# Kernel optimization log

Measured on AMD Instinct MI355X. Metric: run time of the kernel, lower is better.

## Reference

```python
import jax, jax.numpy as jnp
import numpy as np
from jax import lax

B, H, W, D_MODEL = 2, 64, 64, 96
EXPAND = 2
D_INNER = EXPAND * D_MODEL  # 192
D_STATE = 16
D_CONV = 3
DT_RANK = -(-D_MODEL // 16)  # 6 ('auto')
K = 2  # num_direction


def diagonal_order(size):
    # faithful to SCANS 'diagonal': main diag, then upper tri row-major, then lower tri
    locs = [i * size + i for i in range(size)]
    for i in range(size):
        for j in range(i + 1, size):
            locs.append(i * size + j)
    for i in range(size):
        for j in range(i):
            locs.append(i * size + j)
    return np.asarray(locs, dtype=np.int32)

_ORDER = diagonal_order(H)               # encode: gather by locs_flat
_INV_ORDER = np.argsort(_ORDER).astype(np.int32)  # decode: gather by argsort(locs_flat)


def setup_inputs():
    key = jax.random.key(0)
    ks = jax.random.split(key, 8)
    s = 0.02
    return {
        "x": jax.random.normal(ks[0], (B, H, W, D_MODEL), jnp.float32),
        "w_in": jax.random.normal(ks[1], (2 * D_INNER, D_MODEL), jnp.float32) * s,
        "conv_w": jax.random.normal(ks[2], (D_INNER, 1, D_CONV, D_CONV), jnp.float32) * 0.1,
        "conv_b": jnp.zeros((D_INNER,), jnp.float32),
        "x_proj_w": jax.random.normal(ks[3], (K, DT_RANK + 2 * D_STATE, D_INNER), jnp.float32) * s,
        "dt_w": jax.random.uniform(ks[4], (K, D_INNER, DT_RANK), jnp.float32, -(DT_RANK ** -0.5), DT_RANK ** -0.5),
        "dt_b": jax.random.uniform(ks[5], (K, D_INNER), jnp.float32, -4.6, -2.3),  # inv-softplus of dt in [~1e-2,1e-1]
        "A_logs": jnp.tile(jnp.log(jnp.arange(1, D_STATE + 1, dtype=jnp.float32))[None, :], (K * D_INNER, 1)),
        "Ds": jnp.ones((K * D_INNER,), jnp.float32),
        "ln_g": jnp.ones((D_INNER,), jnp.float32),
        "ln_b": jnp.zeros((D_INNER,), jnp.float32),
        "w_out": jax.random.normal(ks[6], (D_MODEL, D_INNER), jnp.float32) * s,
    }


def _selective_scan(xs, dts, A, Bs, Cs, Ds2, dt_bias):
    # xs, dts: (B,K,D,L); A: (K,D,N); Bs, Cs: (B,K,N,L); Ds2, dt_bias: (K,D)
    delta = jax.nn.softplus(dts + dt_bias[None, :, :, None])           # (B,K,D,L)
    dA = jnp.exp(jnp.einsum('bkdl,kdn->lbkdn', delta, A))              # (L,B,K,D,N)
    dBu = jnp.einsum('bkdl,bknl,bkdl->lbkdn', delta, Bs, xs)           # (L,B,K,D,N)
    Ct = jnp.transpose(Cs, (3, 0, 1, 2))                               # (L,B,K,N)

    h0 = jnp.zeros(dA.shape[1:], dA.dtype)                             # (B,K,D,N)

    def step(h, inp):
        a, bu, c = inp
        h = a * h + bu
        y = jnp.einsum('bkdn,bkn->bkd', h, c)
        return h, y

    _, ys = lax.scan(step, h0, (dA, dBu, Ct))                          # ys: (L,B,K,D)
    return jnp.transpose(ys, (1, 2, 3, 0)) + Ds2[None, :, :, None] * xs  # (B,K,D,L)


def reference(x, w_in, conv_w, conv_b, x_proj_w, dt_w, dt_b, A_logs, Ds, ln_g, ln_b, w_out):
    Bsz, Hh, Ww, _ = x.shape
    L = Hh * Ww
    order = jnp.asarray(_ORDER)
    inv = jnp.asarray(_INV_ORDER)

    xz = x @ w_in.T                                   # (B,H,W,2*D_INNER)
    xi, z = jnp.split(xz, 2, axis=-1)

    xc = jnp.transpose(xi, (0, 3, 1, 2))              # (B,D,H,W)
    xc = lax.conv_general_dilated(xc, conv_w, (1, 1), 'SAME',
                                  feature_group_count=D_INNER)
    xc = jax.nn.silu(xc + conv_b[None, :, None, None])

    xf = xc.reshape(Bsz, D_INNER, L)
    xs0 = xf[:, :, order]                             # diagonal-scan encode
    xs = jnp.stack([xs0, xs0[:, :, ::-1]], axis=1)    # (B,K,D,L), fwd + reversed

    x_dbl = jnp.einsum('bkdl,kcd->bkcl', xs, x_proj_w)
    dts, Bs, Cs = jnp.split(x_dbl, [DT_RANK, DT_RANK + D_STATE], axis=2)
    dts = jnp.einsum('bkrl,kdr->bkdl', dts, dt_w)

    A = -jnp.exp(A_logs).reshape(K, D_INNER, D_STATE)
    out_y = _selective_scan(xs, dts, A, Bs, Cs, Ds.reshape(K, D_INNER), dt_b)  # (B,K,D,L)

    y = out_y[:, 0] + out_y[:, 1, :, ::-1]            # un-flip reverse direction, merge
    y = y[:, :, inv]                                  # diagonal-scan decode
    y = jnp.transpose(y, (0, 2, 1)).reshape(Bsz, Hh, Ww, D_INNER)

    mu = jnp.mean(y, axis=-1, keepdims=True)
    var = jnp.var(y, axis=-1, keepdims=True)
    y = (y - mu) * lax.rsqrt(var + 1e-5) * ln_g + ln_b  # out_norm (LayerNorm)

    y = y * jax.nn.silu(z)
    return y @ w_out.T
```

## Files before the change

### kernel.cpp

```cpp
#include <hip/hip_runtime.h>
#include <math.h>

#define BB 2
#define DM 96
#define DI 192
#define DST 16
#define DRK 6
#define LL 4096
#define NCH 128
#define CT 32

__device__ __forceinline__ int inv_ord(int i, int j) {
    if (i == j) return i;
    if (j > i)  return 64 + i * 63 - (i * (i - 1)) / 2 + (j - i - 1);
    return 2080 + (i * (i - 1)) / 2 + j;
}

__device__ __forceinline__ float silu_f(float v) {
    return v / (1.f + __expf(-v));
}

__device__ __forceinline__ float softplus_f(float a) {
    return a > 20.f ? a : __logf(1.f + __expf(a));
}

__global__ __launch_bounds__(256) void k_gemm_in(const float* __restrict__ x,
                                                 const float* __restrict__ w_in,
                                                 float* __restrict__ xi,
                                                 float* __restrict__ zs) {
    __shared__ float aT[96][68];
    __shared__ float bT[96][68];
    const int tid = threadIdx.x;
    const int bm = blockIdx.x, bn = blockIdx.y;

    for (int f = tid; f < 64 * 24; f += 256) {
        int mm = f / 24, k4 = f % 24;
        float4 v = *(const float4*)(x + (size_t)(bm * 64 + mm) * 96 + k4 * 4);
        aT[k4 * 4 + 0][mm] = v.x; aT[k4 * 4 + 1][mm] = v.y;
        aT[k4 * 4 + 2][mm] = v.z; aT[k4 * 4 + 3][mm] = v.w;
    }
    for (int f = tid; f < 64 * 24; f += 256) {
        int nn = f / 24, k4 = f % 24;
        float4 v = *(const float4*)(w_in + (size_t)(bn * 64 + nn) * 96 + k4 * 4);
        bT[k4 * 4 + 0][nn] = v.x; bT[k4 * 4 + 1][nn] = v.y;
        bT[k4 * 4 + 2][nn] = v.z; bT[k4 * 4 + 3][nn] = v.w;
    }
    __syncthreads();

    const int tn = tid & 15, tm = tid >> 4;
    float acc[4][4] = {};
#pragma unroll 4
    for (int k = 0; k < 96; ++k) {
        float4 av = *(const float4*)&aT[k][tm * 4];
        float4 bv = *(const float4*)&bT[k][tn * 4];
        acc[0][0] += av.x * bv.x; acc[0][1] += av.x * bv.y; acc[0][2] += av.x * bv.z; acc[0][3] += av.x * bv.w;
        acc[1][0] += av.y * bv.x; acc[1][1] += av.y * bv.y; acc[1][2] += av.y * bv.z; acc[1][3] += av.y * bv.w;
        acc[2][0] += av.z * bv.x; acc[2][1] += av.z * bv.y; acc[2][2] += av.z * bv.z; acc[2][3] += av.z * bv.w;
        acc[3][0] += av.w * bv.x; acc[3][1] += av.w * bv.y; acc[3][2] += av.w * bv.z; acc[3][3] += av.w * bv.w;
    }

#pragma unroll
    for (int i = 0; i < 4; ++i) {
#pragma unroll
        for (int j = 0; j < 4; ++j) {
            int m = bm * 64 + tm * 4 + i;
            int n = bn * 64 + tn * 4 + j;
            float v = acc[i][j];
            if (n < DI) xi[(size_t)m * DI + n] = v;
            else        zs[(size_t)m * DI + (n - DI)] = silu_f(v);
        }
    }
}

__global__ __launch_bounds__(256) void k_conv(const float* __restrict__ xi,
                                              const float* __restrict__ cw,
                                              const float* __restrict__ cb,
                                              float* __restrict__ xs0) {
    int t = blockIdx.x * 256 + threadIdx.x;
    int c4 = t % 48;
    int p = t / 48;
    int b = p >> 12;
    int hw = p & 4095;
    int i = hw >> 6, j = hw & 63;
    int c = c4 * 4;
    float a0 = cb[c], a1 = cb[c + 1], a2 = cb[c + 2], a3 = cb[c + 3];
#pragma unroll
    for (int kh = -1; kh <= 1; ++kh) {
        int i2 = i + kh;
        if (i2 < 0 || i2 > 63) continue;
#pragma unroll
        for (int kw = -1; kw <= 1; ++kw) {
            int j2 = j + kw;
            if (j2 < 0 || j2 > 63) continue;
            float4 v = *(const float4*)(xi + ((size_t)(b << 12) + (i2 << 6) + j2) * DI + c);
            int wi = (kh + 1) * 3 + (kw + 1);
            a0 += v.x * cw[(c + 0) * 9 + wi];
            a1 += v.y * cw[(c + 1) * 9 + wi];
            a2 += v.z * cw[(c + 2) * 9 + wi];
            a3 += v.w * cw[(c + 3) * 9 + wi];
        }
    }
    a0 = silu_f(a0); a1 = silu_f(a1); a2 = silu_f(a2); a3 = silu_f(a3);
    int m = inv_ord(i, j);
    *(float4*)(xs0 + ((size_t)(b << 12) + m) * DI + c) = make_float4(a0, a1, a2, a3);
}

__global__ __launch_bounds__(512) void k_proj4(const float* __restrict__ xs0,
                                               const float* __restrict__ xpw,
                                               float* __restrict__ t) {
    __shared__ float xa[192 * 65];
    const int tid = threadIdx.x;
    const int rowbase = blockIdx.x * 64;
    const int k = blockIdx.y;

    for (int f = tid; f < 64 * 48; f += 512) {
        int r = f / 48, q4 = f % 48;
        float4 v = *(const float4*)(xs0 + (size_t)(rowbase + r) * DI + q4 * 4);
        xa[(q4 * 4 + 0) * 65 + r] = v.x;
        xa[(q4 * 4 + 1) * 65 + r] = v.y;
        xa[(q4 * 4 + 2) * 65 + r] = v.z;
        xa[(q4 * 4 + 3) * 65 + r] = v.w;
    }
    __syncthreads();

    const int w = __builtin_amdgcn_readfirstlane(tid >> 6);
    const int lane = tid & 63;
    const float* wb = xpw + (size_t)k * 38 * DI;

    float acc[5] = {};
    const float* wr[5];
#pragma unroll
    for (int jj = 0; jj < 5; ++jj) {
        int c = w * 5 + jj; if (c > 37) c = 37;
        wr[jj] = wb + (size_t)c * DI;
    }
#pragma unroll 4
    for (int q = 0; q < DI; ++q) {
        float xv = xa[q * 65 + lane];
#pragma unroll
        for (int jj = 0; jj < 5; ++jj) acc[jj] += wr[jj][q] * xv;
    }
    __syncthreads();

    float* tt = xa;
#pragma unroll
    for (int jj = 0; jj < 5; ++jj) {
        int c = w * 5 + jj;
        tt[c * 65 + lane] = acc[jj];
    }
    __syncthreads();
    for (int f = tid; f < 64 * 38; f += 512) {
        int m = f / 38, c = f % 38;
        float v = tt[c * 65 + m];
        int outc = (k == 0) ? (c < 6 ? 64 + c : c - 6)
                            : (c < 6 ? 70 + c : 26 + c);
        t[(size_t)(rowbase + m) * 80 + outc] = v;
    }
}

__global__ __launch_bounds__(256) void k_scan_a(const float* __restrict__ xs0,
                                                const float* __restrict__ t,
                                                const float* __restrict__ A_logs,
                                                const float* __restrict__ dtw,
                                                const float* __restrict__ dtb,
                                                float* __restrict__ aprod,
                                                float* __restrict__ hend) {
    __shared__ float ld_delta[CT][64];
    __shared__ float ld_x[CT][64];
    __shared__ float ld_B[CT][16];
    const int tid = threadIdx.x;
    int blk = blockIdx.x;
    int c = blk & (NCH - 1);
    int rest = blk >> 7;
    int dthird = rest % 3;
    int bk = rest / 3;
    int b = bk >> 1, k = bk & 1;
    const int koffB = k ? 32 : 0;
    const int doff = 64 + 6 * k;

    if (tid < 128) {
        int r = tid >> 2, q = tid & 3;
        int gl = c * CT + r;
        int msrc = k ? (LL - 1 - gl) : gl;
        size_t rb = (size_t)(b << 12) + msrc;
        float4 v = *(const float4*)(t + rb * 80 + koffB + q * 4);
        *(float4*)&ld_B[r][q * 4] = v;
    }
    {
        int dloc = tid & 63;
        int d = dthird * 64 + dloc;
        const float* dwr = dtw + ((size_t)k * DI + d) * 6;
        float w0 = dwr[0], w1 = dwr[1], w2 = dwr[2];
        float w3 = dwr[3], w4 = dwr[4], w5 = dwr[5];
        float bias = dtb[k * DI + d];
        for (int f = tid; f < CT * 64; f += 256) {
            int r = f >> 6;
            int gl = c * CT + r;
            int msrc = k ? (LL - 1 - gl) : gl;
            size_t rb = (size_t)(b << 12) + msrc;
            ld_x[r][dloc] = xs0[rb * DI + d];
            const float* tr = t + rb * 80 + doff;
            float acc = bias + tr[0] * w0 + tr[1] * w1 + tr[2] * w2
                             + tr[3] * w3 + tr[4] * w4 + tr[5] * w5;
            ld_delta[r][dloc] = softplus_f(acc);
        }
    }
    __syncthreads();

    const int dd = tid >> 2, ng = tid & 3;
    const int d = dthird * 64 + dd;
    float Av0, Av1, Av2, Av3;
    {
        const float* ar = A_logs + ((size_t)k * DI + d) * 16 + ng * 4;
        Av0 = -__expf(ar[0]); Av1 = -__expf(ar[1]);
        Av2 = -__expf(ar[2]); Av3 = -__expf(ar[3]);
    }
    float h0 = 0, h1 = 0, h2 = 0, h3 = 0;
    float p0 = 1, p1 = 1, p2 = 1, p3 = 1;
#pragma unroll 4
    for (int l = 0; l < CT; ++l) {
        float dl = ld_delta[l][dd];
        float dx = dl * ld_x[l][dd];
        float4 bv = *(const float4*)&ld_B[l][ng * 4];
        float a0 = __expf(dl * Av0), a1 = __expf(dl * Av1);
        float a2 = __expf(dl * Av2), a3 = __expf(dl * Av3);
        h0 = a0 * h0 + dx * bv.x; h1 = a1 * h1 + dx * bv.y;
        h2 = a2 * h2 + dx * bv.z; h3 = a3 * h3 + dx * bv.w;
        p0 *= a0; p1 *= a1; p2 *= a2; p3 *= a3;
    }
    size_t o = ((size_t)bk * NCH + c) * 3072 + (size_t)d * 16 + ng * 4;
    *(float4*)(aprod + o) = make_float4(p0, p1, p2, p3);
    *(float4*)(hend + o)  = make_float4(h0, h1, h2, h3);
}

__global__ __launch_bounds__(256) void k_scan_b(const float* __restrict__ aprod,
                                                const float* __restrict__ hend,
                                                float* __restrict__ hinit) {
    int wid = blockIdx.x * 4 + (threadIdx.x >> 6);
    int lane = threadIdx.x & 63;
    int bk = wid / 3072;
    int rr = wid - bk * 3072;
    size_t base = (size_t)bk * NCH * 3072 + rr;

    float a0 = aprod[base + (size_t)lane * 3072];
    float h0 = hend [base + (size_t)lane * 3072];
    float a1 = aprod[base + (size_t)(lane + 64) * 3072];
    float h1 = hend [base + (size_t)(lane + 64) * 3072];

#pragma unroll
    for (int off = 1; off < 64; off <<= 1) {
        float ap = __shfl_up(a0, off), hp = __shfl_up(h0, off);
        if (lane >= off) { h0 = fmaf(a0, hp, h0); a0 *= ap; }
    }
    float he = __shfl_up(h0, 1);
    float hT = __shfl(h0, 63);
    if (lane == 0) he = 0.f;
    hinit[base + (size_t)lane * 3072] = he;

#pragma unroll
    for (int off = 1; off < 64; off <<= 1) {
        float ap = __shfl_up(a1, off), hp = __shfl_up(h1, off);
        if (lane >= off) { h1 = fmaf(a1, hp, h1); a1 *= ap; }
    }
    float ae2 = __shfl_up(a1, 1), he2 = __shfl_up(h1, 1);
    if (lane == 0) { ae2 = 1.f; he2 = 0.f; }
    hinit[base + (size_t)(lane + 64) * 3072] = fmaf(ae2, hT, he2);
}

__global__ __launch_bounds__(256) void k_scan_c(const float* __restrict__ xs0,
                                                const float* __restrict__ t,
                                                const float* __restrict__ A_logs,
                                                const float* __restrict__ dtw,
                                                const float* __restrict__ dtb,
                                                const float* __restrict__ hinit,
                                                float* __restrict__ ya,
                                                float* __restrict__ yb) {
    __shared__ float ld_delta[CT][64];
    __shared__ float ld_x[CT][64];
    __shared__ float ld_B[CT][16];
    __shared__ float ld_C[CT][16];
    __shared__ float ld_y[CT][64];
    const int tid = threadIdx.x;
    int blk = blockIdx.x;
    int c = blk & (NCH - 1);
    int rest = blk >> 7;
    int dthird = rest % 3;
    int bk = rest / 3;
    int b = bk >> 1, k = bk & 1;
    const int koffB = k ? 32 : 0;
    const int doff = 64 + 6 * k;

    {
        int r = tid >> 3, q = tid & 7;
        int gl = c * CT + r;
        int msrc = k ? (LL - 1 - gl) : gl;
        size_t rb = (size_t)(b << 12) + msrc;
        float4 v = *(const float4*)(t + rb * 80 + koffB + q * 4);
        if (q < 4) *(float4*)&ld_B[r][q * 4] = v;
        else       *(float4*)&ld_C[r][(q - 4) * 4] = v;
    }
    {
        int dloc = tid & 63;
        int d = dthird * 64 + dloc;
        const float* dwr = dtw + ((size_t)k * DI + d) * 6;
        float w0 = dwr[0], w1 = dwr[1], w2 = dwr[2];
        float w3 = dwr[3], w4 = dwr[4], w5 = dwr[5];
        float bias = dtb[k * DI + d];
        for (int f = tid; f < CT * 64; f += 256) {
            int r = f >> 6;
            int gl = c * CT + r;
            int msrc = k ? (LL - 1 - gl) : gl;
            size_t rb = (size_t)(b << 12) + msrc;
            ld_x[r][dloc] = xs0[rb * DI + d];
            const float* tr = t + rb * 80 + doff;
            float acc = bias + tr[0] * w0 + tr[1] * w1 + tr[2] * w2
                             + tr[3] * w3 + tr[4] * w4 + tr[5] * w5;
            ld_delta[r][dloc] = softplus_f(acc);
        }
    }
    __syncthreads();

    const int dd = tid >> 2, ng = tid & 3;
    const int d = dthird * 64 + dd;
    float Av0, Av1, Av2, Av3;
    {
        const float* ar = A_logs + ((size_t)k * DI + d) * 16 + ng * 4;
        Av0 = -__expf(ar[0]); Av1 = -__expf(ar[1]);
        Av2 = -__expf(ar[2]); Av3 = -__expf(ar[3]);
    }
    float h0, h1, h2, h3;
    {
        size_t o = ((size_t)bk * NCH + c) * 3072 + (size_t)d * 16 + ng * 4;
        float4 hv = *(const float4*)(hinit + o);
        h0 = hv.x; h1 = hv.y; h2 = hv.z; h3 = hv.w;
    }
#pragma unroll 4
    for (int l = 0; l < CT; ++l) {
        float dl = ld_delta[l][dd];
        float dx = dl * ld_x[l][dd];
        float4 bv = *(const float4*)&ld_B[l][ng * 4];
        float4 cv = *(const float4*)&ld_C[l][ng * 4];
        float a0 = __expf(dl * Av0), a1 = __expf(dl * Av1);
        float a2 = __expf(dl * Av2), a3 = __expf(dl * Av3);
        h0 = a0 * h0 + dx * bv.x; h1 = a1 * h1 + dx * bv.y;
        h2 = a2 * h2 + dx * bv.z; h3 = a3 * h3 + dx * bv.w;
        float p = h0 * cv.x + h1 * cv.y + h2 * cv.z + h3 * cv.w;
        p += __shfl_xor(p, 1);
        p += __shfl_xor(p, 2);
        if (ng == 0) ld_y[l][dd] = p;
    }
    __syncthreads();

    float* ydst = k ? yb : ya;
    for (int f = tid; f < CT * 64; f += 256) {
        int r = f >> 6;
        int dloc = tid & 63;
        int gl = c * CT + r;
        int msrc = k ? (LL - 1 - gl) : gl;
        size_t rb = (size_t)(b << 12) + msrc;
        ydst[rb * DI + dthird * 64 + dloc] = ld_y[r][dloc];
    }
}

__global__ __launch_bounds__(256) void k_out(const float* __restrict__ ya,
                                             const float* __restrict__ yb,
                                             const float* __restrict__ xs0,
                                             const float* __restrict__ Ds,
                                             const float* __restrict__ zs,
                                             const float* __restrict__ ln_g,
                                             const float* __restrict__ ln_b,
                                             const float* __restrict__ w_out,
                                             float* __restrict__ out) {
    __shared__ float lnb[16][200];
    __shared__ float bT[96][104];
    __shared__ float stat[16][2];
    const int tid = threadIdx.x;
    const int pb = blockIdx.x * 16;

    for (int f = tid; f < 16 * 48; f += 256) {
        int r = f / 48, q4 = f % 48;
        int p = pb + r;
        int b = p >> 12, pp = p & 4095;
        int m = inv_ord(pp >> 6, pp & 63);
        size_t rbase = ((size_t)(b << 12) + m) * DI + q4 * 4;
        float4 va = *(const float4*)(ya + rbase);
        float4 vb = *(const float4*)(yb + rbase);
        float4 vx = *(const float4*)(xs0 + rbase);
        float4 d0 = *(const float4*)(Ds + q4 * 4);
        float4 d1 = *(const float4*)(Ds + DI + q4 * 4);
        lnb[r][q4 * 4 + 0] = va.x + vb.x + (d0.x + d1.x) * vx.x;
        lnb[r][q4 * 4 + 1] = va.y + vb.y + (d0.y + d1.y) * vx.y;
        lnb[r][q4 * 4 + 2] = va.z + vb.z + (d0.z + d1.z) * vx.z;
        lnb[r][q4 * 4 + 3] = va.w + vb.w + (d0.w + d1.w) * vx.w;
    }
    __syncthreads();

    if (tid < 128) {
        int r = tid >> 3, sub = tid & 7;
        float s = 0.f, s2 = 0.f;
        for (int q = 0; q < 24; ++q) {
            float v = lnb[r][sub * 24 + q];
            s += v; s2 += v * v;
        }
#pragma unroll
        for (int off = 1; off < 8; off <<= 1) {
            s += __shfl_xor(s, off);
            s2 += __shfl_xor(s2, off);
        }
        if (sub == 0) {
            float mu = s * (1.f / 192.f);
            float var = s2 * (1.f / 192.f) - mu * mu;
            stat[r][0] = mu;
            stat[r][1] = rsqrtf(var + 1e-5f);
        }
    }
    __syncthreads();

    for (int f = tid; f < 16 * 48; f += 256) {
        int r = f / 48, q4 = f % 48;
        int p = pb + r;
        float4 vz = *(const float4*)(zs + (size_t)p * DI + q4 * 4);
        float4 g  = *(const float4*)(ln_g + q4 * 4);
        float4 bb = *(const float4*)(ln_b + q4 * 4);
        float mu = stat[r][0], isd = stat[r][1];
        lnb[r][q4*4+0] = ((lnb[r][q4*4+0] - mu) * isd * g.x + bb.x) * vz.x;
        lnb[r][q4*4+1] = ((lnb[r][q4*4+1] - mu) * isd * g.y + bb.y) * vz.y;
        lnb[r][q4*4+2] = ((lnb[r][q4*4+2] - mu) * isd * g.z + bb.z) * vz.z;
        lnb[r][q4*4+3] = ((lnb[r][q4*4+3] - mu) * isd * g.w + bb.w) * vz.w;
    }

    const int tn = tid & 15, tm = tid >> 4;
    float acc[6] = {};
#pragma unroll
    for (int kt = 0; kt < 2; ++kt) {
        __syncthreads();
        for (int f = tid; f < 96 * 24; f += 256) {
            int nn = f / 24, k4 = f % 24;
            float4 v = *(const float4*)(w_out + (size_t)nn * DI + kt * 96 + k4 * 4);
            bT[k4 * 4 + 0][nn] = v.x; bT[k4 * 4 + 1][nn] = v.y;
            bT[k4 * 4 + 2][nn] = v.z; bT[k4 * 4 + 3][nn] = v.w;
        }
        __syncthreads();
#pragma unroll 4
        for (int kq = 0; kq < 96; ++kq) {
            float av = lnb[tm][kt * 96 + kq];
            float2 b0 = *(const float2*)&bT[kq][tn * 6];
            float2 b1 = *(const float2*)&bT[kq][tn * 6 + 2];
            float2 b2 = *(const float2*)&bT[kq][tn * 6 + 4];
            acc[0] += av * b0.x; acc[1] += av * b0.y;
            acc[2] += av * b1.x; acc[3] += av * b1.y;
            acc[4] += av * b2.x; acc[5] += av * b2.y;
        }
    }
    int p = pb + tm;
#pragma unroll
    for (int j = 0; j < 6; ++j)
        out[(size_t)p * DM + tn * 6 + j] = acc[j];
}

extern "C" void kernel_launch(void* const* d_in, const int* in_sizes, int n_in,
                              void* d_out, int out_size, void* d_ws, size_t ws_size,
                              hipStream_t stream) {
    (void)in_sizes; (void)n_in; (void)out_size; (void)ws_size;
    const float* x      = (const float*)d_in[0];
    const float* w_in   = (const float*)d_in[1];
    const float* conv_w = (const float*)d_in[2];
    const float* conv_b = (const float*)d_in[3];
    const float* xpw    = (const float*)d_in[4];
    const float* dtw    = (const float*)d_in[5];
    const float* dtb    = (const float*)d_in[6];
    const float* A_logs = (const float*)d_in[7];
    const float* Ds     = (const float*)d_in[8];
    const float* ln_g   = (const float*)d_in[9];
    const float* ln_b   = (const float*)d_in[10];
    const float* w_out  = (const float*)d_in[11];
    float* out = (float*)d_out;

    float* ws    = (float*)d_ws;
    float* xi    = ws;
    float* zs    = xi + 1572864;
    float* xs0   = zs + 1572864;
    float* tbuf  = xs0 + 1572864;
    float* aprod = tbuf + 1048576;
    float* hend  = aprod + 1572864;
    float* hinit = hend + 1572864;
    float* ya    = hinit + 1572864;
    float* yb    = ya + 1572864;

    k_gemm_in<<<dim3(128, 6), 256, 0, stream>>>(x, w_in, xi, zs);
    k_conv<<<1536, 256, 0, stream>>>(xi, conv_w, conv_b, xs0);
    k_proj4<<<dim3(128, 2), 512, 0, stream>>>(xs0, xpw, tbuf);
    k_scan_a<<<4 * 3 * NCH, 256, 0, stream>>>(xs0, tbuf, A_logs, dtw, dtb, aprod, hend);
    k_scan_b<<<3072, 256, 0, stream>>>(aprod, hend, hinit);
    k_scan_c<<<4 * 3 * NCH, 256, 0, stream>>>(xs0, tbuf, A_logs, dtw, dtb, hinit, ya, yb);
    k_out<<<512, 256, 0, stream>>>(ya, yb, xs0, Ds, zs, ln_g, ln_b, w_out, out);
}
```

Measured before the change: 146.2 us.

## Transpose chunk carry buffers, precompute delta*x, closed-form decay product, direct y stores

The chunk-end decay product and state are now stored in a chunk-contiguous transposed layout, so the cross-chunk scan kernel reads them with coalesced loads. The decay product is computed as exp(A*sum(delta)) instead of a running product, and delta*x is precomputed once into shared memory. The final scan kernel writes y straight to global from the ng==0 lanes, dropping the shared staging buffer and one barrier. The risk is that the aprodT/hendT writes from scan_a become strided and uncoalesced, and the direct y stores come from only a quarter of the lanes.

```diff
diff --git a/kernel.cpp b/kernel.cpp
--- a/kernel.cpp
+++ b/kernel.cpp
@@ -163,10 +163,10 @@
                                                 const float* __restrict__ A_logs,
                                                 const float* __restrict__ dtw,
                                                 const float* __restrict__ dtb,
-                                                float* __restrict__ aprod,
-                                                float* __restrict__ hend) {
+                                                float* __restrict__ aprodT,
+                                                float* __restrict__ hendT) {
     __shared__ float ld_delta[CT][64];
-    __shared__ float ld_x[CT][64];
+    __shared__ float ld_dx[CT][64];
     __shared__ float ld_B[CT][16];
     const int tid = threadIdx.x;
     int blk = blockIdx.x;
@@ -198,11 +198,12 @@
             int gl = c * CT + r;
             int msrc = k ? (LL - 1 - gl) : gl;
             size_t rb = (size_t)(b << 12) + msrc;
-            ld_x[r][dloc] = xs0[rb * DI + d];
             const float* tr = t + rb * 80 + doff;
             float acc = bias + tr[0] * w0 + tr[1] * w1 + tr[2] * w2
                              + tr[3] * w3 + tr[4] * w4 + tr[5] * w5;
-            ld_delta[r][dloc] = softplus_f(acc);
+            float dl = softplus_f(acc);
+            ld_delta[r][dloc] = dl;
+            ld_dx[r][dloc] = dl * xs0[rb * DI + d];
         }
     }
     __syncthreads();
@@ -216,36 +217,40 @@
         Av2 = -__expf(ar[2]); Av3 = -__expf(ar[3]);
     }
     float h0 = 0, h1 = 0, h2 = 0, h3 = 0;
-    float p0 = 1, p1 = 1, p2 = 1, p3 = 1;
+    float S = 0.f;
 #pragma unroll 4
     for (int l = 0; l < CT; ++l) {
         float dl = ld_delta[l][dd];
-        float dx = dl * ld_x[l][dd];
+        float dx = ld_dx[l][dd];
         float4 bv = *(const float4*)&ld_B[l][ng * 4];
         float a0 = __expf(dl * Av0), a1 = __expf(dl * Av1);
         float a2 = __expf(dl * Av2), a3 = __expf(dl * Av3);
         h0 = a0 * h0 + dx * bv.x; h1 = a1 * h1 + dx * bv.y;
         h2 = a2 * h2 + dx * bv.z; h3 = a3 * h3 + dx * bv.w;
-        p0 *= a0; p1 *= a1; p2 *= a2; p3 *= a3;
-    }
-    size_t o = ((size_t)bk * NCH + c) * 3072 + (size_t)d * 16 + ng * 4;
-    *(float4*)(aprod + o) = make_float4(p0, p1, p2, p3);
-    *(float4*)(hend + o)  = make_float4(h0, h1, h2, h3);
-}
-
-__global__ __launch_bounds__(256) void k_scan_b(const float* __restrict__ aprod,
-                                                const float* __restrict__ hend,
+        S += dl;
+    }
+    float p0 = __expf(Av0 * S), p1 = __expf(Av1 * S);
+    float p2 = __expf(Av2 * S), p3 = __expf(Av3 * S);
+    size_t o = ((size_t)bk * 3072 + (size_t)d * 16 + ng * 4) * 128 + c;
+    aprodT[o]       = p0; hendT[o]       = h0;
+    aprodT[o + 128] = p1; hendT[o + 128] = h1;
+    aprodT[o + 256] = p2; hendT[o + 256] = h2;
+    aprodT[o + 384] = p3; hendT[o + 384] = h3;
+}
+
+__global__ __launch_bounds__(256) void k_scan_b(const float* __restrict__ aprodT,
+                                                const float* __restrict__ hendT,
                                                 float* __restrict__ hinit) {
     int wid = blockIdx.x * 4 + (threadIdx.x >> 6);
     int lane = threadIdx.x & 63;
     int bk = wid / 3072;
     int rr = wid - bk * 3072;
-    size_t base = (size_t)bk * NCH * 3072 + rr;
-
-    float a0 = aprod[base + (size_t)lane * 3072];
-    float h0 = hend [base + (size_t)lane * 3072];
-    float a1 = aprod[base + (size_t)(lane + 64) * 3072];
-    float h1 = hend [base + (size_t)(lane + 64) * 3072];
+    size_t base = ((size_t)bk * 3072 + rr) * 128;
+
+    float a0 = aprodT[base + lane];
+    float h0 = hendT [base + lane];
+    float a1 = aprodT[base + 64 + lane];
+    float h1 = hendT [base + 64 + lane];
 
 #pragma unroll
     for (int off = 1; off < 64; off <<= 1) {
@@ -255,7 +260,8 @@
     float he = __shfl_up(h0, 1);
     float hT = __shfl(h0, 63);
     if (lane == 0) he = 0.f;
-    hinit[base + (size_t)lane * 3072] = he;
+    size_t ob = (size_t)bk * NCH * 3072 + rr;
+    hinit[ob + (size_t)lane * 3072] = he;
 
 #pragma unroll
     for (int off = 1; off < 64; off <<= 1) {
@@ -264,7 +270,7 @@
     }
     float ae2 = __shfl_up(a1, 1), he2 = __shfl_up(h1, 1);
     if (lane == 0) { ae2 = 1.f; he2 = 0.f; }
-    hinit[base + (size_t)(lane + 64) * 3072] = fmaf(ae2, hT, he2);
+    hinit[ob + (size_t)(lane + 64) * 3072] = fmaf(ae2, hT, he2);
 }
 
 __global__ __launch_bounds__(256) void k_scan_c(const float* __restrict__ xs0,
@@ -276,10 +282,9 @@
                                                 float* __restrict__ ya,
                                                 float* __restrict__ yb) {
     __shared__ float ld_delta[CT][64];
-    __shared__ float ld_x[CT][64];
+    __shared__ float ld_dx[CT][64];
     __shared__ float ld_B[CT][16];
     __shared__ float ld_C[CT][16];
-    __shared__ float ld_y[CT][64];
     const int tid = threadIdx.x;
     int blk = blockIdx.x;
     int c = blk & (NCH - 1);
@@ -311,11 +316,12 @@
             int gl = c * CT + r;
             int msrc = k ? (LL - 1 - gl) : gl;
             size_t rb = (size_t)(b << 12) + msrc;
-            ld_x[r][dloc] = xs0[rb * DI + d];
             const float* tr = t + rb * 80 + doff;
             float acc = bias + tr[0] * w0 + tr[1] * w1 + tr[2] * w2
                              + tr[3] * w3 + tr[4] * w4 + tr[5] * w5;
-            ld_delta[r][dloc] = softplus_f(acc);
+            float dl = softplus_f(acc);
+            ld_delta[r][dloc] = dl;
+            ld_dx[r][dloc] = dl * xs0[rb * DI + d];
         }
     }
     __syncthreads();
@@ -334,10 +340,12 @@
         float4 hv = *(const float4*)(hinit + o);
         h0 = hv.x; h1 = hv.y; h2 = hv.z; h3 = hv.w;
     }
+    float* ydst = k ? yb : ya;
+    const size_t bbase = (size_t)(b << 12);
 #pragma unroll 4
     for (int l = 0; l < CT; ++l) {
         float dl = ld_delta[l][dd];
-        float dx = dl * ld_x[l][dd];
+        float dx = ld_dx[l][dd];
         float4 bv = *(const float4*)&ld_B[l][ng * 4];
         float4 cv = *(const float4*)&ld_C[l][ng * 4];
         float a0 = __expf(dl * Av0), a1 = __expf(dl * Av1);
@@ -347,18 +355,11 @@
         float p = h0 * cv.x + h1 * cv.y + h2 * cv.z + h3 * cv.w;
         p += __shfl_xor(p, 1);
         p += __shfl_xor(p, 2);
-        if (ng == 0) ld_y[l][dd] = p;
-    }
-    __syncthreads();
-
-    float* ydst = k ? yb : ya;
-    for (int f = tid; f < CT * 64; f += 256) {
-        int r = f >> 6;
-        int dloc = tid & 63;
-        int gl = c * CT + r;
-        int msrc = k ? (LL - 1 - gl) : gl;
-        size_t rb = (size_t)(b << 12) + msrc;
-        ydst[rb * DI + dthird * 64 + dloc] = ld_y[r][dloc];
+        if (ng == 0) {
+            int gl = c * CT + l;
+            int msrc = k ? (LL - 1 - gl) : gl;
+            ydst[(bbase + msrc) * DI + d] = p;
+        }
     }
 }
 
```

After: 144.4 us. About the same (-1.2%).
